# Performance work log

Measured on AMD Instinct MI355X. Metric: run time of the kernel, lower is better.

The kernel has to match this reference:

```python
import jax, jax.numpy as jnp
import numpy as np

IN_FEATURES = 1024
OUT_FEATURES = 1024
BATCH = 32768
EPS = 1e-6


def setup_inputs() -> dict:
    key = jax.random.key(0)
    kx, kw = jax.random.split(key)
    x = jax.random.normal(kx, (BATCH, IN_FEATURES), dtype=jnp.float32)
    # xavier-uniform-like init for weight [out, in]
    limit = np.sqrt(6.0 / (IN_FEATURES + OUT_FEATURES)).astype(np.float32)
    W = jax.random.uniform(kw, (OUT_FEATURES, IN_FEATURES), dtype=jnp.float32,
                           minval=-limit, maxval=limit)
    b = jnp.zeros((OUT_FEATURES,), dtype=jnp.float32)
    return {"x": x, "W": W, "b": b}


def reference(x, W, b):
    # sign with sign(0) -> +1
    binary_w = jnp.where(W >= 0, 1.0, -1.0).astype(W.dtype)  # [out, in]
    # per-output-row scale, detached in the original (no grad flows through it)
    scale = jnp.maximum(jnp.mean(jnp.abs(W), axis=1, keepdims=True), EPS)  # [out, 1]
    # F.linear(x, binary_w * scale, b) = x @ (binary_w * scale).T + b
    return jnp.einsum('ni,oi->no', x, binary_w * scale) + b
```

## Files before the change

kernel.cpp:

```cpp
#include <hip/hip_runtime.h>


typedef short short8 __attribute__((ext_vector_type(8)));
typedef float f32x4 __attribute__((ext_vector_type(4)));

#define BATCH 32768
#define IN_F  1024
#define OUT_F 1024
#define EPS   1e-6f

#define BM 128
#define BN 128

__device__ __forceinline__ ushort f2bf(float f) {
  unsigned u = __builtin_bit_cast(unsigned, f);
  u += 0x7FFFu + ((u >> 16) & 1u);
  return (ushort)(u >> 16);
}

__device__ __forceinline__ void gload_lds16(const void* g, void* l) {
  __builtin_amdgcn_global_load_lds(
      (const __attribute__((address_space(1))) unsigned*)g,
      (__attribute__((address_space(3))) unsigned*)l, 16, 0, 0);
}

__global__ void bin_kernel(const float* __restrict__ W,
                           ushort* __restrict__ Wb,
                           float* __restrict__ scale) {
  int row = blockIdx.x * 4 + (threadIdx.x >> 6);
  int t = threadIdx.x & 63;
  const float4* wr = (const float4*)(W + (size_t)row * IN_F);
  ushort4* wb = (ushort4*)(Wb + (size_t)row * IN_F);
  float s = 0.f;
#pragma unroll
  for (int i = 0; i < 4; ++i) {
    float4 v = wr[i * 64 + t];
    ushort4 u;
    u.x = (v.x >= 0.f) ? 0x3F80 : 0xBF80;
    u.y = (v.y >= 0.f) ? 0x3F80 : 0xBF80;
    u.z = (v.z >= 0.f) ? 0x3F80 : 0xBF80;
    u.w = (v.w >= 0.f) ? 0x3F80 : 0xBF80;
    wb[i * 64 + t] = u;
    s += fabsf(v.x) + fabsf(v.y) + fabsf(v.z) + fabsf(v.w);
  }
#pragma unroll
  for (int o = 32; o > 0; o >>= 1) s += __shfl_down(s, o);
  if (t == 0) scale[row] = fmaxf(s * (1.0f / (float)IN_F), EPS);
}

__global__ void cvt_kernel(const float* __restrict__ X,
                           ushort* __restrict__ Xb) {
  size_t idx = (size_t)blockIdx.x * 256 + threadIdx.x;
  float4 v = ((const float4*)X)[idx];
  ushort4 u;
  u.x = f2bf(v.x); u.y = f2bf(v.y); u.z = f2bf(v.z); u.w = f2bf(v.w);
  ((ushort4*)Xb)[idx] = u;
}

__global__ void gemm_fast(const ushort* __restrict__ Xb,
                          const ushort* __restrict__ Wb,
                          const float* __restrict__ scale,
                          const float* __restrict__ bias,
                          float* __restrict__ out) {
  __shared__ __align__(16) ushort lA[BM * 64];
  __shared__ __align__(16) ushort lB[BN * 64];

  int bid = blockIdx.x;
  int g = (bid & 7) * 256 + (bid >> 3);
  int mt = g >> 3;
  int nt = g & 7;
  int rowBase = mt * BM;
  int colBase = nt * BN;

  int t = threadIdx.x;
  int lane = t & 63;
  int wave = t >> 6;
  int wr = wave >> 1;
  int wc = wave & 1;

  int srow = (lane >> 3);
  int scol = (lane & 7) * 8;
  const ushort* gA = Xb + (size_t)(rowBase + wave * 8 + srow) * IN_F + scol;
  const ushort* gB = Wb + (size_t)(colBase + wave * 8 + srow) * IN_F + scol;
  ushort* lA_base = &lA[(wave * 8) * 64];
  ushort* lB_base = &lB[(wave * 8) * 64];

  f32x4 acc[4][4];
#pragma unroll
  for (int m = 0; m < 4; ++m)
#pragma unroll
    for (int n = 0; n < 4; ++n) acc[m][n] = (f32x4){0.f, 0.f, 0.f, 0.f};

  for (int kk = 0; kk < IN_F / 64; ++kk) {
    int k0 = kk * 64;
    __syncthreads();

#pragma unroll
    for (int j = 0; j < 4; ++j) {
      gload_lds16(gA + k0 + (size_t)j * 32 * IN_F, lA_base + j * 32 * 64);
      gload_lds16(gB + k0 + (size_t)j * 32 * IN_F, lB_base + j * 32 * 64);
    }
    __syncthreads();

    short8 af[4][2], bfx[4][2];
#pragma unroll
    for (int m = 0; m < 4; ++m)
#pragma unroll
      for (int ks = 0; ks < 2; ++ks) {
        int row = wr * 64 + m * 16 + (lane & 15);
        af[m][ks] = *(const short8*)(&lA[row * 64 + ks * 32 + (lane >> 4) * 8]);
      }
#pragma unroll
    for (int n = 0; n < 4; ++n)
#pragma unroll
      for (int ks = 0; ks < 2; ++ks) {
        int row = wc * 64 + n * 16 + (lane & 15);
        bfx[n][ks] = *(const short8*)(&lB[row * 64 + ks * 32 + (lane >> 4) * 8]);
      }
#pragma unroll
    for (int ks = 0; ks < 2; ++ks)
#pragma unroll
      for (int m = 0; m < 4; ++m)
#pragma unroll
        for (int n = 0; n < 4; ++n)
          acc[m][n] = __builtin_amdgcn_mfma_f32_16x16x32_bf16(
              af[m][ks], bfx[n][ks], acc[m][n], 0, 0, 0);
  }

#pragma unroll
  for (int n = 0; n < 4; ++n) {
    int col = colBase + wc * 64 + n * 16 + (lane & 15);
    float sc = scale[col];
    float bs = bias[col];
#pragma unroll
    for (int m = 0; m < 4; ++m) {
      int r0 = rowBase + wr * 64 + m * 16 + ((lane >> 4) << 2);
#pragma unroll
      for (int j = 0; j < 4; ++j) {
        out[(size_t)(r0 + j) * OUT_F + col] = acc[m][n][j] * sc + bs;
      }
    }
  }
}

__global__ void gemm_kernel(const float* __restrict__ X,
                            const ushort* __restrict__ Wb,
                            const float* __restrict__ scale,
                            const float* __restrict__ bias,
                            float* __restrict__ out) {
  __shared__ __align__(16) ushort lA[BM * 32];
  __shared__ __align__(16) ushort lB[BN * 32];

  int bid = blockIdx.x;
  int g = (bid & 7) * 256 + (bid >> 3);
  int mt = g >> 3;
  int nt = g & 7;
  int rowBase = mt * BM;
  int colBase = nt * BN;

  int t = threadIdx.x;
  int lane = t & 63;
  int wave = t >> 6;
  int wr = wave >> 1;
  int wc = wave & 1;

  f32x4 acc[4][4];
#pragma unroll
  for (int m = 0; m < 4; ++m)
#pragma unroll
    for (int n = 0; n < 4; ++n) acc[m][n] = (f32x4){0.f, 0.f, 0.f, 0.f};

  for (int kk = 0; kk < IN_F / 32; ++kk) {
    int k0 = kk * 32;
    __syncthreads();
#pragma unroll
    for (int i = 0; i < 2; ++i) {
      int idx = t + 256 * i;
      int r = idx >> 2, c16 = idx & 3;
      const float4* gp =
          (const float4*)(X + (size_t)(rowBase + r) * IN_F + k0 + c16 * 8);
      float4 v0 = gp[0];
      float4 v1 = gp[1];
      short8 u;
      u[0] = (short)f2bf(v0.x); u[1] = (short)f2bf(v0.y);
      u[2] = (short)f2bf(v0.z); u[3] = (short)f2bf(v0.w);
      u[4] = (short)f2bf(v1.x); u[5] = (short)f2bf(v1.y);
      u[6] = (short)f2bf(v1.z); u[7] = (short)f2bf(v1.w);
      int off = (r * 32 + c16 * 8) ^ ((r & 7) << 3);
      *(short8*)(&lA[off]) = u;
    }
#pragma unroll
    for (int i = 0; i < 2; ++i) {
      int idx = t + 256 * i;
      int r = idx >> 2, c16 = idx & 3;
      const short8* gp =
          (const short8*)(Wb + (size_t)(colBase + r) * IN_F + k0 + c16 * 8);
      short8 u = *gp;
      int off = (r * 32 + c16 * 8) ^ ((r & 7) << 3);
      *(short8*)(&lB[off]) = u;
    }
    __syncthreads();

    short8 af[4], bfr[4];
#pragma unroll
    for (int m = 0; m < 4; ++m) {
      int r = wr * 64 + m * 16 + (lane & 15);
      int off = (r * 32 + (lane >> 4) * 8) ^ ((r & 7) << 3);
      af[m] = *(const short8*)(&lA[off]);
    }
#pragma unroll
    for (int n = 0; n < 4; ++n) {
      int r = wc * 64 + n * 16 + (lane & 15);
      int off = (r * 32 + (lane >> 4) * 8) ^ ((r & 7) << 3);
      bfr[n] = *(const short8*)(&lB[off]);
    }
#pragma unroll
    for (int m = 0; m < 4; ++m)
#pragma unroll
      for (int n = 0; n < 4; ++n)
        acc[m][n] = __builtin_amdgcn_mfma_f32_16x16x32_bf16(
            af[m], bfr[n], acc[m][n], 0, 0, 0);
  }

#pragma unroll
  for (int n = 0; n < 4; ++n) {
    int col = colBase + wc * 64 + n * 16 + (lane & 15);
    float sc = scale[col];
    float bs = bias[col];
#pragma unroll
    for (int m = 0; m < 4; ++m) {
      int r0 = rowBase + wr * 64 + m * 16 + ((lane >> 4) << 2);
#pragma unroll
      for (int j = 0; j < 4; ++j) {
        out[(size_t)(r0 + j) * OUT_F + col] = acc[m][n][j] * sc + bs;
      }
    }
  }
}

extern "C" void kernel_launch(void* const* d_in, const int* in_sizes, int n_in,
                              void* d_out, int out_size, void* d_ws,
                              size_t ws_size, hipStream_t stream) {
  const float* x = (const float*)d_in[0];
  const float* W = (const float*)d_in[1];
  const float* b = (const float*)d_in[2];
  float* out = (float*)d_out;

  float* scale = (float*)d_ws;
  ushort* Wb = (ushort*)((char*)d_ws + 4096);
  ushort* xb = (ushort*)((char*)d_ws + 4096 + 2097152);
  const size_t need = 4096 + 2097152 + (size_t)BATCH * IN_F * 2;

  bin_kernel<<<OUT_F / 4, 256, 0, stream>>>(W, Wb, scale);

  dim3 grid((BATCH / BM) * (OUT_F / BN));
  if (ws_size >= need) {
    cvt_kernel<<<(BATCH * IN_F / 4) / 256, 256, 0, stream>>>(x, xb);
    gemm_fast<<<grid, 256, 0, stream>>>(xb, Wb, scale, b, out);
  } else {
    gemm_kernel<<<grid, 256, 0, stream>>>(x, Wb, scale, b, out);
  }
}
```

Measured before the change: 302.6 us.

## Replace bf16 GEMM with 256x256-tile, 8-wave, double-buffered ping-pong pipeline

Swaps the 128x128, 4-wave GEMM for a 256x256-tile kernel with 8 waves and 128 KB of LDS. It double-buffers K tiles with direct global-to-LDS loads and an XOR-swizzled layout. Global loads for upcoming K tiles are interleaved with MFMA sections under explicit barriers and s_setprio, so memory traffic overlaps compute and LDS bank conflicts drop. The larger tile increases reuse per byte loaded. The cost is heavy register pressure (a 128-entry accumulator), hand-tuned vmcnt waits that are fragile, and fewer blocks per CU.

```diff
diff --git a/kernel.cpp b/kernel.cpp
--- a/kernel.cpp
+++ b/kernel.cpp
@@ -8,9 +8,6 @@
 #define IN_F  1024
 #define OUT_F 1024
 #define EPS   1e-6f
-
-#define BM 128
-#define BN 128
 
 __device__ __forceinline__ ushort f2bf(float f) {
   unsigned u = __builtin_bit_cast(unsigned, f);
@@ -57,90 +54,140 @@
   ((ushort4*)Xb)[idx] = u;
 }
 
-__global__ void gemm_fast(const ushort* __restrict__ Xb,
-                          const ushort* __restrict__ Wb,
-                          const float* __restrict__ scale,
-                          const float* __restrict__ bias,
-                          float* __restrict__ out) {
-  __shared__ __align__(16) ushort lA[BM * 64];
-  __shared__ __align__(16) ushort lB[BN * 64];
+__device__ __forceinline__ void rd4(short8 (*dst)[2], const char* base,
+                                    int c0, int c1) {
+#pragma unroll
+  for (int m = 0; m < 4; ++m) {
+    dst[m][0] = *(const short8*)(base + m * 2048 + c0);
+    dst[m][1] = *(const short8*)(base + m * 2048 + c1);
+  }
+}
+__device__ __forceinline__ void rd2(short8 (*dst)[2], const char* base,
+                                    int c0, int c1) {
+#pragma unroll
+  for (int n = 0; n < 2; ++n) {
+    dst[n][0] = *(const short8*)(base + n * 2048 + c0);
+    dst[n][1] = *(const short8*)(base + n * 2048 + c1);
+  }
+}
+template <int MB, int NB>
+__device__ __forceinline__ void mmq(f32x4 (*acc)[4], const short8 (*a)[2],
+                                    const short8 (*b)[2]) {
+#pragma unroll
+  for (int ks = 0; ks < 2; ++ks)
+#pragma unroll
+    for (int m = 0; m < 4; ++m)
+#pragma unroll
+      for (int n = 0; n < 2; ++n)
+        acc[MB + m][NB + n] = __builtin_amdgcn_mfma_f32_16x16x32_bf16(
+            a[m][ks], b[n][ks], acc[MB + m][NB + n], 0, 0, 0);
+}
+
+#define FENCE() do { __builtin_amdgcn_sched_barrier(0); \
+                     asm volatile("" ::: "memory"); } while (0)
+#define BAR()   do { FENCE(); __builtin_amdgcn_s_barrier(); FENCE(); } while (0)
+#define MFMA_SEC(stmt) do { BAR(); __builtin_amdgcn_s_setprio(1); stmt; \
+                            __builtin_amdgcn_s_setprio(0); BAR(); } while (0)
+
+__global__ __launch_bounds__(512, 2) void gemm8p(
+    const ushort* __restrict__ Xb, const ushort* __restrict__ Wb,
+    const float* __restrict__ scale, const float* __restrict__ bias,
+    float* __restrict__ out) {
+  __shared__ __align__(16) char L[131072];
 
   int bid = blockIdx.x;
-  int g = (bid & 7) * 256 + (bid >> 3);
-  int mt = g >> 3;
-  int nt = g & 7;
-  int rowBase = mt * BM;
-  int colBase = nt * BN;
-
-  int t = threadIdx.x;
-  int lane = t & 63;
-  int wave = t >> 6;
-  int wr = wave >> 1;
-  int wc = wave & 1;
-
-  int srow = (lane >> 3);
-  int scol = (lane & 7) * 8;
-  const ushort* gA = Xb + (size_t)(rowBase + wave * 8 + srow) * IN_F + scol;
-  const ushort* gB = Wb + (size_t)(colBase + wave * 8 + srow) * IN_F + scol;
-  ushort* lA_base = &lA[(wave * 8) * 64];
-  ushort* lB_base = &lB[(wave * 8) * 64];
-
-  f32x4 acc[4][4];
-#pragma unroll
-  for (int m = 0; m < 4; ++m)
+  int g = (bid & 7) * 64 + (bid >> 3);
+  int mt = g >> 2, nt = g & 3;
+  int rowBase = mt * 256, colBase = nt * 256;
+
+  int tid = threadIdx.x, lane = tid & 63, w = tid >> 6;
+  int wm = w >> 2, wn = w & 3;
+
+  int baseA = (wm * 128 + (lane & 15)) * 128;
+  int baseB = 65536 + (wn * 64 + (lane & 15)) * 128;
+  int c0 = ((lane >> 4) * 16) ^ ((lane & 7) << 4);
+  int c1 = c0 ^ 64;
+  int srl = lane >> 3;
+  int scb = ((lane & 7) ^ srl) * 8;
+  int bu0 = (w & 3) * 8 + (w >> 2) * 64;
+  const ushort* gA = Xb + ((size_t)rowBase + srl) * IN_F + scb;
+  const ushort* gB = Wb + ((size_t)colBase + srl) * IN_F + scb;
+
+#define STA(bufOff, kt, row0) \
+  gload_lds16(gA + (size_t)(row0) * IN_F + (kt) * 64, L + (bufOff) + (row0) * 128)
+#define STB(bufOff, kt, row0) \
+  gload_lds16(gB + (size_t)(row0) * IN_F + (kt) * 64, \
+              L + 65536 + (bufOff) + (row0) * 128)
+
+  f32x4 acc[8][4];
+#pragma unroll
+  for (int m = 0; m < 8; ++m)
 #pragma unroll
     for (int n = 0; n < 4; ++n) acc[m][n] = (f32x4){0.f, 0.f, 0.f, 0.f};
 
-  for (int kk = 0; kk < IN_F / 64; ++kk) {
-    int k0 = kk * 64;
-    __syncthreads();
-
-#pragma unroll
-    for (int j = 0; j < 4; ++j) {
-      gload_lds16(gA + k0 + (size_t)j * 32 * IN_F, lA_base + j * 32 * 64);
-      gload_lds16(gB + k0 + (size_t)j * 32 * IN_F, lB_base + j * 32 * 64);
-    }
-    __syncthreads();
-
-    short8 af[4][2], bfx[4][2];
-#pragma unroll
-    for (int m = 0; m < 4; ++m)
-#pragma unroll
-      for (int ks = 0; ks < 2; ++ks) {
-        int row = wr * 64 + m * 16 + (lane & 15);
-        af[m][ks] = *(const short8*)(&lA[row * 64 + ks * 32 + (lane >> 4) * 8]);
-      }
-#pragma unroll
-    for (int n = 0; n < 4; ++n)
-#pragma unroll
-      for (int ks = 0; ks < 2; ++ks) {
-        int row = wc * 64 + n * 16 + (lane & 15);
-        bfx[n][ks] = *(const short8*)(&lB[row * 64 + ks * 32 + (lane >> 4) * 8]);
-      }
-#pragma unroll
-    for (int ks = 0; ks < 2; ++ks)
-#pragma unroll
-      for (int m = 0; m < 4; ++m)
-#pragma unroll
-        for (int n = 0; n < 4; ++n)
-          acc[m][n] = __builtin_amdgcn_mfma_f32_16x16x32_bf16(
-              af[m][ks], bfx[n][ks], acc[m][n], 0, 0, 0);
-  }
+  STA(0, 0, w * 8);        STA(0, 0, 128 + w * 8);
+  STA(0, 0, 64 + w * 8);   STA(0, 0, 192 + w * 8);
+  STB(0, 0, bu0);          STB(0, 0, bu0 + 128);
+  STB(0, 0, bu0 + 32);     STB(0, 0, bu0 + 160);
+  STA(32768, 1, w * 8);      STA(32768, 1, 128 + w * 8);
+  STA(32768, 1, 64 + w * 8); STA(32768, 1, 192 + w * 8);
+  STB(32768, 1, bu0);        STB(32768, 1, bu0 + 128);
+  STB(32768, 1, bu0 + 32);   STB(32768, 1, bu0 + 160);
+  asm volatile("s_waitcnt vmcnt(8)");
+  BAR();
+
+  short8 aLo[4][2], aHi[4][2], bb[2][2];
+
+  for (int it = 0; it < 8; ++it) {
+    int kt2 = (2 * it + 2) & 15;
+    int kt3 = (2 * it + 3) & 15;
+
+    rd4(aLo, L + baseA, c0, c1);
+    rd2(bb, L + baseB, c0, c1);
+    MFMA_SEC((mmq<0, 0>(acc, aLo, bb)));
+    rd4(aHi, L + baseA + 4 * 2048, c0, c1);
+    STA(0, kt2, w * 8); STA(0, kt2, 128 + w * 8);
+    MFMA_SEC((mmq<4, 0>(acc, aHi, bb)));
+    rd2(bb, L + baseB + 2 * 2048, c0, c1);
+    STB(0, kt2, bu0); STB(0, kt2, bu0 + 128);
+    MFMA_SEC((mmq<4, 2>(acc, aHi, bb)));
+    STA(0, kt2, 64 + w * 8); STA(0, kt2, 192 + w * 8);
+    asm volatile("s_waitcnt vmcnt(6)");
+    MFMA_SEC((mmq<0, 2>(acc, aLo, bb)));
+
+    rd4(aLo, L + 32768 + baseA, c0, c1);
+    rd2(bb, L + 32768 + baseB, c0, c1);
+    STB(0, kt2, bu0 + 32); STB(0, kt2, bu0 + 160);
+    MFMA_SEC((mmq<0, 0>(acc, aLo, bb)));
+    rd4(aHi, L + 32768 + baseA + 4 * 2048, c0, c1);
+    STA(32768, kt3, w * 8); STA(32768, kt3, 128 + w * 8);
+    MFMA_SEC((mmq<4, 0>(acc, aHi, bb)));
+    rd2(bb, L + 32768 + baseB + 2 * 2048, c0, c1);
+    STB(32768, kt3, bu0); STB(32768, kt3, bu0 + 128);
+    MFMA_SEC((mmq<4, 2>(acc, aHi, bb)));
+    STA(32768, kt3, 64 + w * 8); STA(32768, kt3, 192 + w * 8);
+    STB(32768, kt3, bu0 + 32);   STB(32768, kt3, bu0 + 160);
+    asm volatile("s_waitcnt vmcnt(6)");
+    MFMA_SEC((mmq<0, 2>(acc, aLo, bb)));
+  }
+
+  asm volatile("s_waitcnt vmcnt(0)");
 
 #pragma unroll
   for (int n = 0; n < 4; ++n) {
-    int col = colBase + wc * 64 + n * 16 + (lane & 15);
+    int col = colBase + wn * 64 + n * 16 + (lane & 15);
     float sc = scale[col];
     float bs = bias[col];
 #pragma unroll
-    for (int m = 0; m < 4; ++m) {
-      int r0 = rowBase + wr * 64 + m * 16 + ((lane >> 4) << 2);
-#pragma unroll
-      for (int j = 0; j < 4; ++j) {
+    for (int m = 0; m < 8; ++m) {
+      int r0 = rowBase + wm * 128 + m * 16 + ((lane >> 4) << 2);
+#pragma unroll
+      for (int j = 0; j < 4; ++j)
         out[(size_t)(r0 + j) * OUT_F + col] = acc[m][n][j] * sc + bs;
-      }
-    }
-  }
+    }
+  }
+#undef STA
+#undef STB
 }
 
 __global__ void gemm_kernel(const float* __restrict__ X,
@@ -148,28 +195,19 @@
                             const float* __restrict__ scale,
                             const float* __restrict__ bias,
                             float* __restrict__ out) {
-  __shared__ __align__(16) ushort lA[BM * 32];
-  __shared__ __align__(16) ushort lB[BN * 32];
-
+  __shared__ __align__(16) ushort lA[128 * 32];
+  __shared__ __align__(16) ushort lB[128 * 32];
   int bid = blockIdx.x;
   int g = (bid & 7) * 256 + (bid >> 3);
-  int mt = g >> 3;
-  int nt = g & 7;
-  int rowBase = mt * BM;
-  int colBase = nt * BN;
-
-  int t = threadIdx.x;
-  int lane = t & 63;
-  int wave = t >> 6;
-  int wr = wave >> 1;
-  int wc = wave & 1;
-
+  int mt = g >> 3, nt = g & 7;
+  int rowBase = mt * 128, colBase = nt * 128;
+  int t = threadIdx.x, lane = t & 63, wave = t >> 6;
+  int wr = wave >> 1, wc = wave & 1;
   f32x4 acc[4][4];
 #pragma unroll
   for (int m = 0; m < 4; ++m)
 #pragma unroll
     for (int n = 0; n < 4; ++n) acc[m][n] = (f32x4){0.f, 0.f, 0.f, 0.f};
-
   for (int kk = 0; kk < IN_F / 32; ++kk) {
     int k0 = kk * 32;
     __syncthreads();
@@ -188,19 +226,11 @@
       u[6] = (short)f2bf(v1.z); u[7] = (short)f2bf(v1.w);
       int off = (r * 32 + c16 * 8) ^ ((r & 7) << 3);
       *(short8*)(&lA[off]) = u;
-    }
-#pragma unroll
-    for (int i = 0; i < 2; ++i) {
-      int idx = t + 256 * i;
-      int r = idx >> 2, c16 = idx & 3;
-      const short8* gp =
+      const short8* gp2 =
           (const short8*)(Wb + (size_t)(colBase + r) * IN_F + k0 + c16 * 8);
-      short8 u = *gp;
-      int off = (r * 32 + c16 * 8) ^ ((r & 7) << 3);
-      *(short8*)(&lB[off]) = u;
+      *(short8*)(&lB[off]) = *gp2;
     }
     __syncthreads();
-
     short8 af[4], bfr[4];
 #pragma unroll
     for (int m = 0; m < 4; ++m) {
@@ -221,7 +251,6 @@
         acc[m][n] = __builtin_amdgcn_mfma_f32_16x16x32_bf16(
             af[m], bfr[n], acc[m][n], 0, 0, 0);
   }
-
 #pragma unroll
   for (int n = 0; n < 4; ++n) {
     int col = colBase + wc * 64 + n * 16 + (lane & 15);
@@ -231,9 +260,8 @@
     for (int m = 0; m < 4; ++m) {
       int r0 = rowBase + wr * 64 + m * 16 + ((lane >> 4) << 2);
 #pragma unroll
-      for (int j = 0; j < 4; ++j) {
+      for (int j = 0; j < 4; ++j)
         out[(size_t)(r0 + j) * OUT_F + col] = acc[m][n][j] * sc + bs;
-      }
     }
   }
 }
@@ -253,11 +281,12 @@
 
   bin_kernel<<<OUT_F / 4, 256, 0, stream>>>(W, Wb, scale);
 
-  dim3 grid((BATCH / BM) * (OUT_F / BN));
   if (ws_size >= need) {
     cvt_kernel<<<(BATCH * IN_F / 4) / 256, 256, 0, stream>>>(x, xb);
-    gemm_fast<<<grid, 256, 0, stream>>>(xb, Wb, scale, b, out);
+    gemm8p<<<(BATCH / 256) * (OUT_F / 256), 512, 0, stream>>>(xb, Wb, scale,
+                                                              b, out);
   } else {
-    gemm_kernel<<<grid, 256, 0, stream>>>(x, Wb, scale, b, out);
-  }
-}
+    gemm_kernel<<<(BATCH / 128) * (OUT_F / 128), 256, 0, stream>>>(
+        x, Wb, scale, b, out);
+  }
+}
```

Measured after the change: 298.3 us. Within noise of the previous version (-1.4%).
